# Performance work log

Measured on AMD Instinct MI355X. Metric: run time of the kernel, lower is better.

## Reference

```python
import jax, jax.numpy as jnp
import numpy as np

B, S, D, H = 2, 2048, 1024, 16
DK = D // H


def setup_inputs() -> dict:
    key = jax.random.key(0)
    ks = jax.random.split(key, 12)
    sc = 1.0 / np.sqrt(D)
    inp = {
        "q": jax.random.normal(ks[0], (B, S, D), jnp.float32),
        "k": jax.random.normal(ks[1], (B, S, D), jnp.float32),
        "v": jax.random.normal(ks[2], (B, S, D), jnp.float32),
        # causal mask, broadcastable over batch and heads
        "mask": jnp.tril(jnp.ones((S, S), jnp.int32))[None, None],
        "Wq": jax.random.normal(ks[3], (D, D), jnp.float32) * sc,
        "bq": jax.random.normal(ks[4], (D,), jnp.float32) * 0.02,
        "Wk": jax.random.normal(ks[5], (D, D), jnp.float32) * sc,
        "bk": jax.random.normal(ks[6], (D,), jnp.float32) * 0.02,
        "Wv": jax.random.normal(ks[7], (D, D), jnp.float32) * sc,
        "bv": jax.random.normal(ks[8], (D,), jnp.float32) * 0.02,
        "Wo": jax.random.normal(ks[9], (D, D), jnp.float32) * sc,
        "bo": jax.random.normal(ks[10], (D,), jnp.float32) * 0.02,
    }
    return inp


def reference(q, k, v, mask, Wq, bq, Wk, bk, Wv, bv, Wo, bo):
    b, s, _ = q.shape
    # QKV projections (torch Linear: x @ W.T + b)
    qh = (q @ Wq.T + bq).reshape(b, s, H, DK).transpose(0, 2, 1, 3)  # [B,H,S,DK]
    kh = (k @ Wk.T + bk).reshape(b, -1, H, DK).transpose(0, 2, 1, 3)
    vh = (v @ Wv.T + bv).reshape(b, -1, H, DK).transpose(0, 2, 1, 3)
    scores = jnp.einsum("bhqd,bhkd->bhqk", qh, kh) / np.sqrt(DK)  # [B,H,S,S]
    scores = jnp.where(mask == 0, jnp.float32(-1e9), scores)
    attn = jax.nn.softmax(scores, axis=-1)
    # dropout p=0.0 (eval) -> identity
    x = jnp.einsum("bhqk,bhkd->bhqd", attn, vh)  # [B,H,S,DK]
    x = x.transpose(0, 2, 1, 3).reshape(b, s, H * DK)
    return x @ Wo.T + bo
```

## Files before the change

### kernel.cpp

```cpp
#include <hip/hip_runtime.h>
#include <hip/hip_bf16.h>
#include <cstdint>
#include <cstddef>

using u16   = unsigned short;
using u32   = uint32_t;
using u16x4 = __attribute__((ext_vector_type(4))) unsigned short;
using u16x8 = __attribute__((ext_vector_type(8))) unsigned short;
using s16x8 = __attribute__((ext_vector_type(8))) short;
using f32x4 = __attribute__((ext_vector_type(4))) float;
using f32x16 = __attribute__((ext_vector_type(16))) float;

#define B_DIM  2
#define S_DIM  2048
#define D_DIM  1024
#define H_DIM  16
#define DK_DIM 64

__device__ __forceinline__ u16 f2bf(float f) {
  union { float f; uint32_t u; } c; c.f = f;
  uint32_t u = c.u;
  return (u16)((u + 0x7FFFu + ((u >> 16) & 1u)) >> 16);
}
__device__ __forceinline__ float bf2f(u16 v) {
  union { uint32_t u; float f; } c; c.u = (uint32_t)v << 16;
  return c.f;
}

__device__ __forceinline__ void gload16(const void* g, void* l) {
  __builtin_amdgcn_global_load_lds(
      (const __attribute__((address_space(1))) void*)g,
      (__attribute__((address_space(3))) void*)l, 16, 0, 0);
}

__device__ __forceinline__ int chunk_base(int qt) {
  return (qt < 4) ? qt
       : (qt < 8) ? 4 + 2 * (qt - 4)
       : (qt < 12) ? 12 + 3 * (qt - 8)
       : 24 + 4 * (qt - 12);
}

__global__ __launch_bounds__(256) void cast_bf16_kernel(
    const float* s0, const float* s1, const float* s2, const float* s3,
    u16* d0, u16* d1, u16* d2, u16* d3, int n)
{
  const float* s; u16* d;
  switch (blockIdx.y) {
    case 0: s = s0; d = d0; break;
    case 1: s = s1; d = d1; break;
    case 2: s = s2; d = d2; break;
    default: s = s3; d = d3; break;
  }
  int i = (blockIdx.x * 256 + threadIdx.x) * 8;
  if (i >= n) return;
  f32x4 a = *(const f32x4*)(s + i);
  f32x4 b = *(const f32x4*)(s + i + 4);
  u16x8 ov;
  ov[0] = f2bf(a[0]); ov[1] = f2bf(a[1]); ov[2] = f2bf(a[2]); ov[3] = f2bf(a[3]);
  ov[4] = f2bf(b[0]); ov[5] = f2bf(b[1]); ov[6] = f2bf(b[2]); ov[7] = f2bf(b[3]);
  *(u16x8*)(d + i) = ov;
}

#define BM 128
#define BN 128
#define BK 64

__device__ __forceinline__ void gemm_bt_core(
    const u16* __restrict__ A, const u16* __restrict__ W,
    const float* __restrict__ bias, void* __restrict__ out, int mode,
    int mtile, int ntile, float oscale)
{
  __shared__ u16 Alds[BM * BK];
  __shared__ u16 Blds[BN * BK];
  const int K = 1024;
  const int tid = threadIdx.x;
  const int w = tid >> 6, l = tid & 63;
  const int lr = l & 15, lg = l >> 4;
  const int wr = w >> 1, wc = w & 1;
  const int m0 = mtile * BM, n0 = ntile * BN;

  f32x4 acc[4][4] = {};

  for (int kt = 0; kt < K / BK; ++kt) {
    const int k0 = kt * BK;
    #pragma unroll
    for (int i = 0; i < 4; ++i) {
      int c = i * 256 + tid;
      int r = c >> 3;
      int cb = ((c & 7) << 4) ^ ((r & 7) << 4);
      gload16((const char*)(A + (size_t)(m0 + r) * K + k0) + cb,
              (char*)Alds + i * 4096 + w * 1024);
    }
    #pragma unroll
    for (int i = 0; i < 4; ++i) {
      int c = i * 256 + tid;
      int r = c >> 3;
      int cb = ((c & 7) << 4) ^ ((r & 7) << 4);
      gload16((const char*)(W + (size_t)(n0 + r) * K + k0) + cb,
              (char*)Blds + i * 4096 + w * 1024);
    }
    __syncthreads();
    #pragma unroll
    for (int ks = 0; ks < 2; ++ks) {
      s16x8 af[4], bf[4];
      #pragma unroll
      for (int mi = 0; mi < 4; ++mi) {
        int r = wr * 64 + mi * 16 + lr;
        int kb = (ks * 64 + lg * 16) ^ ((r & 7) << 4);
        af[mi] = *(const s16x8*)((const char*)Alds + r * 128 + kb);
      }
      #pragma unroll
      for (int ni = 0; ni < 4; ++ni) {
        int r = wc * 64 + ni * 16 + lr;
        int kb = (ks * 64 + lg * 16) ^ ((r & 7) << 4);
        bf[ni] = *(const s16x8*)((const char*)Blds + r * 128 + kb);
      }
      #pragma unroll
      for (int mi = 0; mi < 4; ++mi)
        #pragma unroll
        for (int ni = 0; ni < 4; ++ni)
          acc[mi][ni] = __builtin_amdgcn_mfma_f32_16x16x32_bf16(
              af[mi], bf[ni], acc[mi][ni], 0, 0, 0);
    }
    __syncthreads();
  }

  const int mbase = m0 + wr * 64 + lg * 4;
  const int nbase = n0 + wc * 64 + lr;
  #pragma unroll
  for (int ni = 0; ni < 4; ++ni) {
    int n = nbase + ni * 16;
    float bb = bias[n];
    #pragma unroll
    for (int mi = 0; mi < 4; ++mi) {
      int mr = mbase + mi * 16;
      f32x4 vv = acc[mi][ni];
      if (mode == 2) {
        float* o = (float*)out;
        #pragma unroll
        for (int r = 0; r < 4; ++r) o[(size_t)(mr + r) * 1024 + n] = vv[r] + bb;
      } else if (mode == 0) {
        u16* o = (u16*)out;
        #pragma unroll
        for (int r = 0; r < 4; ++r)
          o[(size_t)(mr + r) * 1024 + n] = f2bf((vv[r] + bb) * oscale);
      } else {
        u16* o = (u16*)out;
        int b = mr >> 11, s = mr & (S_DIM - 1);
        int h = n >> 6, dk = n & 63;
        u16x4 pk;
        #pragma unroll
        for (int r = 0; r < 4; ++r) pk[r] = f2bf(vv[r] + bb);
        *(u16x4*)(o + ((size_t)((b * H_DIM + h) * DK_DIM + dk) * S_DIM + s)) = pk;
      }
    }
  }
}

__global__ __launch_bounds__(256) void qkv_gemm_kernel(
    const u16* xq, const u16* xk, const u16* xv,
    const u16* wq, const u16* wk, const u16* wv,
    const float* bq, const float* bk, const float* bv,
    u16* qlin, u16* klin, u16* vt)
{
  const int f = blockIdx.x;
  const int xcd = f & 7;
  const int s = f >> 3;
  const int z = s >> 5;
  const int r = s & 31;
  const int mtile = xcd * 4 + (r >> 3);
  const int ntile = r & 7;

  const u16* A = (z == 0) ? xq : (z == 1) ? xk : xv;
  const u16* W = (z == 0) ? wq : (z == 1) ? wk : wv;
  const float* bias = (z == 0) ? bq : (z == 1) ? bk : bv;
  void* out = (z == 0) ? (void*)qlin : (z == 1) ? (void*)klin : (void*)vt;
  gemm_bt_core(A, W, bias, out, (z == 2) ? 1 : 0, mtile, ntile,
               (z == 0) ? 0.125f * 1.44269504f : 1.0f);
}

__global__ __launch_bounds__(256) void oproj_kernel(
    const u16* aout, const u16* wo, const float* bo, float* out)
{
  const int f = blockIdx.x;
  const int xcd = f & 7;
  const int s = f >> 3;
  const int mtile = xcd * 4 + (s >> 3);
  const int ntile = s & 7;
  gemm_bt_core(aout, wo, bo, (void*)out, 2, mtile, ntile, 1.0f);
}

__global__ __launch_bounds__(256, 4) void attn_kernel(
    const u16* __restrict__ qlin, const u16* __restrict__ klin,
    const u16* __restrict__ vt, u16* __restrict__ opart,
    float* __restrict__ lpart)
{
  __shared__ u16 Klds[2][8 * 512];
  __shared__ u16 Vlds[2][8 * 512];
  const int tid = threadIdx.x;
  const int w = tid >> 6, l = tid & 63;
  const int lq = l & 31, hi = l >> 5;

  const int f = blockIdx.x;
  const int bh = f & 31;
  const int g = f >> 5;
  int qt, ch;
  if (g < 16)      { qt = 15 - (g >> 2);        ch = g & 3; }
  else if (g < 28) { qt = 11 - (g - 16) / 3;    ch = (g - 16) % 3; }
  else if (g < 36) { qt = 7 - ((g - 28) >> 1);  ch = (g - 28) & 1; }
  else             { qt = 3 - (g - 36);         ch = 0; }
  const int T  = 2 * qt + 2;
  const int nc = (T + 7) >> 3;
  const int jlo = (ch * T) / nc;
  const int jhi = ((ch + 1) * T) / nc;
  const int b = bh >> 4, h = bh & 15;

  const int qb  = qt * 128 + w * 32;
  const int myq = qb + lq;
  const int jtend_w = (qb + 31) >> 6;

  s16x8 qf[4];
  {
    const u16* qptr = qlin + (size_t)(b * S_DIM + myq) * D_DIM + h * DK_DIM + hi * 8;
    #pragma unroll
    for (int db = 0; db < 4; ++db) qf[db] = *(const s16x8*)(qptr + db * 16);
  }

  const u16* kg = klin + (size_t)b * S_DIM * D_DIM + h * DK_DIM;
  const u16* vg = vt + (size_t)(b * H_DIM + h) * DK_DIM * S_DIM;

  f32x16 o0 = {}, o1 = {};
  float l_run = 0.f;

  auto stage = [&](int buf, int jt) {
    const int j0 = jt * 64;
    #pragma unroll
    for (int i = 0; i < 2; ++i) {
      int fk = w * 2 + i;
      int db = fk >> 1, rh = fk & 1;
      gload16(kg + (size_t)(j0 + rh * 32 + lq) * D_DIM + db * 16 + hi * 8,
              (char*)&Klds[buf][0] + fk * 1024);
      gload16(vg + (size_t)(rh * 32 + lq) * S_DIM + j0 + db * 16 + hi * 8,
              (char*)&Vlds[buf][0] + fk * 1024);
    }
  };

  stage(0, jlo);

  #pragma unroll 1
  for (int jt = jlo; jt < jhi; ++jt) {
    const int cur = (jt - jlo) & 1;
    asm volatile("s_waitcnt vmcnt(0)" ::: "memory");
    __builtin_amdgcn_s_barrier();
    __builtin_amdgcn_sched_barrier(0);
    if (jt + 1 < jhi) stage(cur ^ 1, jt + 1);

    if (jt <= jtend_w) {
      const int j0 = jt * 64;
      const char* Kb = (const char*)&Klds[cur][0];
      const char* Vb = (const char*)&Vlds[cur][0];

      f32x16 s0 = {}, s1 = {};
      #pragma unroll
      for (int db = 0; db < 4; ++db) {
        s16x8 k0 = *(const s16x8*)(Kb + (db * 2 + 0) * 1024 + l * 16);
        s16x8 k1 = *(const s16x8*)(Kb + (db * 2 + 1) * 1024 + l * 16);
        s0 = __builtin_amdgcn_mfma_f32_32x32x16_bf16(k0, qf[db], s0, 0, 0, 0);
        s1 = __builtin_amdgcn_mfma_f32_32x32x16_bf16(k1, qf[db], s1, 0, 0, 0);
      }

      if (j0 + 63 > qb) {
        #pragma unroll
        for (int r = 0; r < 16; ++r) {
          int kr = (r & 3) + 8 * (r >> 2) + 4 * hi;
          if (j0 + kr > myq)      s0[r] = -1e30f;
          if (j0 + 32 + kr > myq) s1[r] = -1e30f;
        }
      }

      u32 wds[16];
      float ls = 0.f;
      #pragma unroll
      for (int i = 0; i < 8; ++i) {
        float pa = __builtin_amdgcn_exp2f(s0[2 * i]);
        float pb = __builtin_amdgcn_exp2f(s0[2 * i + 1]);
        ls += pa + pb;
        wds[i] = (u32)f2bf(pa) | ((u32)f2bf(pb) << 16);
        float pc = __builtin_amdgcn_exp2f(s1[2 * i]);
        float pd = __builtin_amdgcn_exp2f(s1[2 * i + 1]);
        ls += pc + pd;
        wds[8 + i] = (u32)f2bf(pc) | ((u32)f2bf(pd) << 16);
      }
      l_run += ls;

      #pragma unroll
      for (int ks = 0; ks < 4; ++ks) {
        u32 w0 = wds[4 * ks], w1 = wds[4 * ks + 1];
        u32 w2 = wds[4 * ks + 2], w3 = wds[4 * ks + 3];
        u32 ta = __shfl_xor(hi ? w0 : w2, 32);
        u32 tb = __shfl_xor(hi ? w1 : w3, 32);
        union { u32 u[4]; s16x8 v; } pf;
        pf.u[0] = hi ? ta : w0;
        pf.u[1] = hi ? tb : w1;
        pf.u[2] = hi ? w2 : ta;
        pf.u[3] = hi ? w3 : tb;
        s16x8 v0 = *(const s16x8*)(Vb + (ks * 2 + 0) * 1024 + l * 16);
        s16x8 v1 = *(const s16x8*)(Vb + (ks * 2 + 1) * 1024 + l * 16);
        o0 = __builtin_amdgcn_mfma_f32_32x32x16_bf16(v0, pf.v, o0, 0, 0, 0);
        o1 = __builtin_amdgcn_mfma_f32_32x32x16_bf16(v1, pf.v, o1, 0, 0, 0);
      }
    }
  }

  const size_t gslot = (size_t)bh * 40 + chunk_base(qt) + ch;
  u16* ob = opart + ((gslot * 128) + w * 32 + lq) * 64;
  #pragma unroll
  for (int rq = 0; rq < 4; ++rq) {
    u16x4 pk0, pk1;
    #pragma unroll
    for (int j = 0; j < 4; ++j) {
      pk0[j] = f2bf(o0[rq * 4 + j]);
      pk1[j] = f2bf(o1[rq * 4 + j]);
    }
    *(u16x4*)(ob + rq * 8 + hi * 4)      = pk0;
    *(u16x4*)(ob + 32 + rq * 8 + hi * 4) = pk1;
  }
  float lt = l_run + __shfl_xor(l_run, 32);
  if (hi == 0) lpart[gslot * 128 + w * 32 + lq] = lt;
}

__global__ __launch_bounds__(256) void attn_combine_kernel(
    const u16* __restrict__ opart, const float* __restrict__ lpart,
    u16* __restrict__ aout)
{
  const int f = blockIdx.x;
  const int bh = f & 31, qt = f >> 5;
  const int b = bh >> 4, h = bh & 15;
  const int nc = (2 * qt + 9) >> 3;
  const int cs = chunk_base(qt);

  const int t = threadIdx.x;
  const int row = t >> 1, dbase = (t & 1) * 32;
  float acc[32] = {};
  float lsum = 0.f;
  for (int c = 0; c < nc; ++c) {
    const size_t slot = (size_t)bh * 40 + cs + c;
    const u16* pr = opart + ((slot * 128) + row) * 64 + dbase;
    #pragma unroll
    for (int v4 = 0; v4 < 4; ++v4) {
      u16x8 vv = *(const u16x8*)(pr + v4 * 8);
      #pragma unroll
      for (int j = 0; j < 8; ++j) acc[v4 * 8 + j] += bf2f(vv[j]);
    }
    lsum += lpart[slot * 128 + row];
  }
  float inv = 1.f / lsum;
  u16* orow = aout + ((size_t)b * S_DIM + qt * 128 + row) * D_DIM + h * 64 + dbase;
  #pragma unroll
  for (int v4 = 0; v4 < 4; ++v4) {
    u16x8 ov;
    #pragma unroll
    for (int j = 0; j < 8; ++j) ov[j] = f2bf(acc[v4 * 8 + j] * inv);
    *(u16x8*)(orow + v4 * 8) = ov;
  }
}

extern "C" void kernel_launch(void* const* d_in, const int* in_sizes, int n_in,
                              void* d_out, int out_size, void* d_ws, size_t ws_size,
                              hipStream_t stream)
{
  (void)in_sizes; (void)n_in; (void)out_size; (void)ws_size;
  const float* q  = (const float*)d_in[0];
  const float* k  = (const float*)d_in[1];
  const float* v  = (const float*)d_in[2];
  const float* Wq = (const float*)d_in[4];
  const float* bq = (const float*)d_in[5];
  const float* Wk = (const float*)d_in[6];
  const float* bk = (const float*)d_in[7];
  const float* Wv = (const float*)d_in[8];
  const float* bv = (const float*)d_in[9];
  const float* Wo = (const float*)d_in[10];
  const float* bo = (const float*)d_in[11];
  float* out = (float*)d_out;

  const size_t XSZ = (size_t)B_DIM * S_DIM * D_DIM;
  const size_t WSZ = (size_t)D_DIM * D_DIM;

  u16* p = (u16*)d_ws;
  u16* qbf  = p; p += XSZ;
  u16* kbf  = p; p += XSZ;
  u16* vbf  = p; p += XSZ;
  u16* wqb  = p; p += WSZ;
  u16* wkb  = p; p += WSZ;
  u16* wvb  = p; p += WSZ;
  u16* wob  = p; p += WSZ;
  u16* qlin = p; p += XSZ;
  u16* klin = p; p += XSZ;
  u16* vtb  = p; p += XSZ;
  u16* aoutb = p; p += XSZ;

  u16*   opart = (u16*)d_ws;
  float* lpart = (float*)((char*)d_ws + (size_t)1280 * 128 * 64 * 2);

  cast_bf16_kernel<<<dim3((unsigned)(XSZ / 8 / 256), 3), 256, 0, stream>>>(
      q, k, v, nullptr, qbf, kbf, vbf, nullptr, (int)XSZ);
  cast_bf16_kernel<<<dim3((unsigned)(WSZ / 8 / 256), 4), 256, 0, stream>>>(
      Wq, Wk, Wv, Wo, wqb, wkb, wvb, wob, (int)WSZ);
  qkv_gemm_kernel<<<768, 256, 0, stream>>>(
      qbf, kbf, vbf, wqb, wkb, wvb, bq, bk, bv, qlin, klin, vtb);
  attn_kernel<<<1280, 256, 0, stream>>>(qlin, klin, vtb, opart, lpart);
  attn_combine_kernel<<<512, 256, 0, stream>>>(opart, lpart, aoutb);
  oproj_kernel<<<256, 256, 0, stream>>>(aoutb, wob, bo, out);
}
```

Before: 134.3 us.

## Double-buffer GEMM LDS with fragment-major layout and K-step of 32

```diff
diff --git a/kernel.cpp b/kernel.cpp
--- a/kernel.cpp
+++ b/kernel.cpp
@@ -63,16 +63,16 @@
 
 #define BM 128
 #define BN 128
-#define BK 64
 
 __device__ __forceinline__ void gemm_bt_core(
     const u16* __restrict__ A, const u16* __restrict__ W,
     const float* __restrict__ bias, void* __restrict__ out, int mode,
     int mtile, int ntile, float oscale)
 {
-  __shared__ u16 Alds[BM * BK];
-  __shared__ u16 Blds[BN * BK];
+  __shared__ u16 Afr[2][8 * 512];
+  __shared__ u16 Wfr[2][8 * 512];
   const int K = 1024;
+  const int NT = K / 32;
   const int tid = threadIdx.x;
   const int w = tid >> 6, l = tid & 63;
   const int lr = l & 15, lg = l >> 4;
@@ -81,48 +81,45 @@
 
   f32x4 acc[4][4] = {};
 
-  for (int kt = 0; kt < K / BK; ++kt) {
-    const int k0 = kt * BK;
+  auto stage = [&](int buf, int kt) {
+    const int k0 = kt * 32;
     #pragma unroll
     for (int i = 0; i < 4; ++i) {
-      int c = i * 256 + tid;
-      int r = c >> 3;
-      int cb = ((c & 7) << 4) ^ ((r & 7) << 4);
-      gload16((const char*)(A + (size_t)(m0 + r) * K + k0) + cb,
-              (char*)Alds + i * 4096 + w * 1024);
-    }
-    #pragma unroll
-    for (int i = 0; i < 4; ++i) {
-      int c = i * 256 + tid;
-      int r = c >> 3;
-      int cb = ((c & 7) << 4) ^ ((r & 7) << 4);
-      gload16((const char*)(W + (size_t)(n0 + r) * K + k0) + cb,
-              (char*)Blds + i * 4096 + w * 1024);
-    }
-    __syncthreads();
-    #pragma unroll
-    for (int ks = 0; ks < 2; ++ks) {
-      s16x8 af[4], bf[4];
+      int fid = w * 4 + i;
+      if (fid < 8) {
+        gload16(A + (size_t)(m0 + fid * 16 + lr) * K + k0 + lg * 8,
+                (char*)&Afr[buf][fid * 512]);
+      } else {
+        int fb = fid - 8;
+        gload16(W + (size_t)(n0 + fb * 16 + lr) * K + k0 + lg * 8,
+                (char*)&Wfr[buf][fb * 512]);
+      }
+    }
+  };
+
+  stage(0, 0);
+
+  #pragma unroll 1
+  for (int kt = 0; kt < NT; ++kt) {
+    const int cur = kt & 1;
+    asm volatile("s_waitcnt vmcnt(0)" ::: "memory");
+    __builtin_amdgcn_s_barrier();
+    __builtin_amdgcn_sched_barrier(0);
+    if (kt + 1 < NT) stage(cur ^ 1, kt + 1);
+
+    s16x8 af[4], bf[4];
+    #pragma unroll
+    for (int mi = 0; mi < 4; ++mi)
+      af[mi] = *(const s16x8*)(&Afr[cur][(wr * 4 + mi) * 512] + (size_t)l * 8);
+    #pragma unroll
+    for (int ni = 0; ni < 4; ++ni)
+      bf[ni] = *(const s16x8*)(&Wfr[cur][(wc * 4 + ni) * 512] + (size_t)l * 8);
+    #pragma unroll
+    for (int mi = 0; mi < 4; ++mi)
       #pragma unroll
-      for (int mi = 0; mi < 4; ++mi) {
-        int r = wr * 64 + mi * 16 + lr;
-        int kb = (ks * 64 + lg * 16) ^ ((r & 7) << 4);
-        af[mi] = *(const s16x8*)((const char*)Alds + r * 128 + kb);
-      }
-      #pragma unroll
-      for (int ni = 0; ni < 4; ++ni) {
-        int r = wc * 64 + ni * 16 + lr;
-        int kb = (ks * 64 + lg * 16) ^ ((r & 7) << 4);
-        bf[ni] = *(const s16x8*)((const char*)Blds + r * 128 + kb);
-      }
-      #pragma unroll
-      for (int mi = 0; mi < 4; ++mi)
-        #pragma unroll
-        for (int ni = 0; ni < 4; ++ni)
-          acc[mi][ni] = __builtin_amdgcn_mfma_f32_16x16x32_bf16(
-              af[mi], bf[ni], acc[mi][ni], 0, 0, 0);
-    }
-    __syncthreads();
+      for (int ni = 0; ni < 4; ++ni)
+        acc[mi][ni] = __builtin_amdgcn_mfma_f32_16x16x32_bf16(
+            af[mi], bf[ni], acc[mi][ni], 0, 0, 0);
   }
 
   const int mbase = m0 + wr * 64 + lg * 4;
@@ -157,7 +154,7 @@
   }
 }
 
-__global__ __launch_bounds__(256) void qkv_gemm_kernel(
+__global__ __launch_bounds__(256, 4) void qkv_gemm_kernel(
     const u16* xq, const u16* xk, const u16* xv,
     const u16* wq, const u16* wk, const u16* wv,
     const float* bq, const float* bk, const float* bv,
@@ -179,7 +176,7 @@
                (z == 0) ? 0.125f * 1.44269504f : 1.0f);
 }
 
-__global__ __launch_bounds__(256) void oproj_kernel(
+__global__ __launch_bounds__(256, 4) void oproj_kernel(
     const u16* aout, const u16* wo, const float* bo, float* out)
 {
   const int f = blockIdx.x;
```

After: 145.3 us. 1.08x slower.

## Store K and V in MFMA fragment order and load directly to registers

Applied to the files above, without the earlier changes.

```diff
diff --git a/kernel.cpp b/kernel.cpp
--- a/kernel.cpp
+++ b/kernel.cpp
@@ -144,14 +144,30 @@
         #pragma unroll
         for (int r = 0; r < 4; ++r)
           o[(size_t)(mr + r) * 1024 + n] = f2bf((vv[r] + bb) * oscale);
+      } else if (mode == 3) {
+        u16* o = (u16*)out;
+        int h = n >> 6, d = n & 63;
+        int db = d >> 4, hi8 = (d >> 3) & 1, e = d & 7;
+        int bb_ = mr >> 11, j = mr & (S_DIM - 1);
+        int jt = j >> 6, rh = (j >> 5) & 1, lq0 = j & 31;
+        size_t base = (((size_t)(bb_ * H_DIM + h) * 32 + jt) * 8 + (db * 2 + rh))
+                      * 512 + (size_t)(hi8 * 32) * 8 + e;
+        #pragma unroll
+        for (int r = 0; r < 4; ++r)
+          o[base + (size_t)(lq0 + r) * 8] = f2bf(vv[r] + bb);
       } else {
         u16* o = (u16*)out;
-        int b = mr >> 11, s = mr & (S_DIM - 1);
         int h = n >> 6, dk = n & 63;
+        int rh = dk >> 5, lq = dk & 31;
+        int bb_ = mr >> 11, j = mr & (S_DIM - 1);
+        int jt = j >> 6, jj = j & 63;
+        int db = jj >> 4, hi8 = (jj >> 3) & 1, e0 = jj & 7;
+        size_t base = (((size_t)(bb_ * H_DIM + h) * 32 + jt) * 8 + (db * 2 + rh))
+                      * 512 + (size_t)(hi8 * 32 + lq) * 8 + e0;
         u16x4 pk;
         #pragma unroll
         for (int r = 0; r < 4; ++r) pk[r] = f2bf(vv[r] + bb);
-        *(u16x4*)(o + ((size_t)((b * H_DIM + h) * DK_DIM + dk) * S_DIM + s)) = pk;
+        *(u16x4*)(o + base) = pk;
       }
     }
   }
@@ -161,7 +177,7 @@
     const u16* xq, const u16* xk, const u16* xv,
     const u16* wq, const u16* wk, const u16* wv,
     const float* bq, const float* bk, const float* bv,
-    u16* qlin, u16* klin, u16* vt)
+    u16* qlin, u16* kfragb, u16* vfragb)
 {
   const int f = blockIdx.x;
   const int xcd = f & 7;
@@ -174,8 +190,8 @@
   const u16* A = (z == 0) ? xq : (z == 1) ? xk : xv;
   const u16* W = (z == 0) ? wq : (z == 1) ? wk : wv;
   const float* bias = (z == 0) ? bq : (z == 1) ? bk : bv;
-  void* out = (z == 0) ? (void*)qlin : (z == 1) ? (void*)klin : (void*)vt;
-  gemm_bt_core(A, W, bias, out, (z == 2) ? 1 : 0, mtile, ntile,
+  void* out = (z == 0) ? (void*)qlin : (z == 1) ? (void*)kfragb : (void*)vfragb;
+  gemm_bt_core(A, W, bias, out, (z == 0) ? 0 : (z == 1) ? 3 : 1, mtile, ntile,
                (z == 0) ? 0.125f * 1.44269504f : 1.0f);
 }
 
@@ -191,12 +207,10 @@
 }
 
 __global__ __launch_bounds__(256, 4) void attn_kernel(
-    const u16* __restrict__ qlin, const u16* __restrict__ klin,
-    const u16* __restrict__ vt, u16* __restrict__ opart,
+    const u16* __restrict__ qlin, const u16* __restrict__ kfrag,
+    const u16* __restrict__ vfrag, u16* __restrict__ opart,
     float* __restrict__ lpart)
 {
-  __shared__ u16 Klds[2][8 * 512];
-  __shared__ u16 Vlds[2][8 * 512];
   const int tid = threadIdx.x;
   const int w = tid >> 6, l = tid & 63;
   const int lq = l & 31, hi = l >> 5;
@@ -218,6 +232,7 @@
   const int qb  = qt * 128 + w * 32;
   const int myq = qb + lq;
   const int jtend_w = (qb + 31) >> 6;
+  const int jend = (jhi < jtend_w + 1) ? jhi : (jtend_w + 1);
 
   s16x8 qf[4];
   {
@@ -226,89 +241,69 @@
     for (int db = 0; db < 4; ++db) qf[db] = *(const s16x8*)(qptr + db * 16);
   }
 
-  const u16* kg = klin + (size_t)b * S_DIM * D_DIM + h * DK_DIM;
-  const u16* vg = vt + (size_t)(b * H_DIM + h) * DK_DIM * S_DIM;
-
   f32x16 o0 = {}, o1 = {};
   float l_run = 0.f;
 
-  auto stage = [&](int buf, int jt) {
+  #pragma unroll 1
+  for (int jt = jlo; jt < jend; ++jt) {
     const int j0 = jt * 64;
-    #pragma unroll
-    for (int i = 0; i < 2; ++i) {
-      int fk = w * 2 + i;
-      int db = fk >> 1, rh = fk & 1;
-      gload16(kg + (size_t)(j0 + rh * 32 + lq) * D_DIM + db * 16 + hi * 8,
-              (char*)&Klds[buf][0] + fk * 1024);
-      gload16(vg + (size_t)(rh * 32 + lq) * S_DIM + j0 + db * 16 + hi * 8,
-              (char*)&Vlds[buf][0] + fk * 1024);
-    }
-  };
-
-  stage(0, jlo);
-
-  #pragma unroll 1
-  for (int jt = jlo; jt < jhi; ++jt) {
-    const int cur = (jt - jlo) & 1;
-    asm volatile("s_waitcnt vmcnt(0)" ::: "memory");
-    __builtin_amdgcn_s_barrier();
-    __builtin_amdgcn_sched_barrier(0);
-    if (jt + 1 < jhi) stage(cur ^ 1, jt + 1);
-
-    if (jt <= jtend_w) {
-      const int j0 = jt * 64;
-      const char* Kb = (const char*)&Klds[cur][0];
-      const char* Vb = (const char*)&Vlds[cur][0];
-
-      f32x16 s0 = {}, s1 = {};
+    const u16* kb = kfrag + ((size_t)bh * 32 + jt) * 8 * 512;
+    const u16* vb = vfrag + ((size_t)bh * 32 + jt) * 8 * 512;
+
+    s16x8 kf2[8];
+    #pragma unroll
+    for (int fk = 0; fk < 8; ++fk)
+      kf2[fk] = *(const s16x8*)(kb + fk * 512 + (size_t)l * 8);
+
+    f32x16 s0 = {}, s1 = {};
+    #pragma unroll
+    for (int db = 0; db < 4; ++db) {
+      s0 = __builtin_amdgcn_mfma_f32_32x32x16_bf16(kf2[db * 2 + 0], qf[db], s0, 0, 0, 0);
+      s1 = __builtin_amdgcn_mfma_f32_32x32x16_bf16(kf2[db * 2 + 1], qf[db], s1, 0, 0, 0);
+    }
+
+    s16x8 vf2[8];
+    #pragma unroll
+    for (int fk = 0; fk < 8; ++fk)
+      vf2[fk] = *(const s16x8*)(vb + fk * 512 + (size_t)l * 8);
+
+    if (j0 + 63 > qb) {
       #pragma unroll
-      for (int db = 0; db < 4; ++db) {
-        s16x8 k0 = *(const s16x8*)(Kb + (db * 2 + 0) * 1024 + l * 16);
-        s16x8 k1 = *(const s16x8*)(Kb + (db * 2 + 1) * 1024 + l * 16);
-        s0 = __builtin_amdgcn_mfma_f32_32x32x16_bf16(k0, qf[db], s0, 0, 0, 0);
-        s1 = __builtin_amdgcn_mfma_f32_32x32x16_bf16(k1, qf[db], s1, 0, 0, 0);
+      for (int r = 0; r < 16; ++r) {
+        int kr = (r & 3) + 8 * (r >> 2) + 4 * hi;
+        if (j0 + kr > myq)      s0[r] = -1e30f;
+        if (j0 + 32 + kr > myq) s1[r] = -1e30f;
       }
-
-      if (j0 + 63 > qb) {
-        #pragma unroll
-        for (int r = 0; r < 16; ++r) {
-          int kr = (r & 3) + 8 * (r >> 2) + 4 * hi;
-          if (j0 + kr > myq)      s0[r] = -1e30f;
-          if (j0 + 32 + kr > myq) s1[r] = -1e30f;
-        }
-      }
-
-      u32 wds[16];
-      float ls = 0.f;
-      #pragma unroll
-      for (int i = 0; i < 8; ++i) {
-        float pa = __builtin_amdgcn_exp2f(s0[2 * i]);
-        float pb = __builtin_amdgcn_exp2f(s0[2 * i + 1]);
-        ls += pa + pb;
-        wds[i] = (u32)f2bf(pa) | ((u32)f2bf(pb) << 16);
-        float pc = __builtin_amdgcn_exp2f(s1[2 * i]);
-        float pd = __builtin_amdgcn_exp2f(s1[2 * i + 1]);
-        ls += pc + pd;
-        wds[8 + i] = (u32)f2bf(pc) | ((u32)f2bf(pd) << 16);
-      }
-      l_run += ls;
-
-      #pragma unroll
-      for (int ks = 0; ks < 4; ++ks) {
-        u32 w0 = wds[4 * ks], w1 = wds[4 * ks + 1];
-        u32 w2 = wds[4 * ks + 2], w3 = wds[4 * ks + 3];
-        u32 ta = __shfl_xor(hi ? w0 : w2, 32);
-        u32 tb = __shfl_xor(hi ? w1 : w3, 32);
-        union { u32 u[4]; s16x8 v; } pf;
-        pf.u[0] = hi ? ta : w0;
-        pf.u[1] = hi ? tb : w1;
-        pf.u[2] = hi ? w2 : ta;
-        pf.u[3] = hi ? w3 : tb;
-        s16x8 v0 = *(const s16x8*)(Vb + (ks * 2 + 0) * 1024 + l * 16);
-        s16x8 v1 = *(const s16x8*)(Vb + (ks * 2 + 1) * 1024 + l * 16);
-        o0 = __builtin_amdgcn_mfma_f32_32x32x16_bf16(v0, pf.v, o0, 0, 0, 0);
-        o1 = __builtin_amdgcn_mfma_f32_32x32x16_bf16(v1, pf.v, o1, 0, 0, 0);
-      }
+    }
+
+    u32 wds[16];
+    float ls = 0.f;
+    #pragma unroll
+    for (int i = 0; i < 8; ++i) {
+      float pa = __builtin_amdgcn_exp2f(s0[2 * i]);
+      float pb = __builtin_amdgcn_exp2f(s0[2 * i + 1]);
+      ls += pa + pb;
+      wds[i] = (u32)f2bf(pa) | ((u32)f2bf(pb) << 16);
+      float pc = __builtin_amdgcn_exp2f(s1[2 * i]);
+      float pd = __builtin_amdgcn_exp2f(s1[2 * i + 1]);
+      ls += pc + pd;
+      wds[8 + i] = (u32)f2bf(pc) | ((u32)f2bf(pd) << 16);
+    }
+    l_run += ls;
+
+    #pragma unroll
+    for (int ks = 0; ks < 4; ++ks) {
+      u32 w0 = wds[4 * ks], w1 = wds[4 * ks + 1];
+      u32 w2 = wds[4 * ks + 2], w3 = wds[4 * ks + 3];
+      u32 ta = __shfl_xor(hi ? w0 : w2, 32);
+      u32 tb = __shfl_xor(hi ? w1 : w3, 32);
+      union { u32 u[4]; s16x8 v; } pf;
+      pf.u[0] = hi ? ta : w0;
+      pf.u[1] = hi ? tb : w1;
+      pf.u[2] = hi ? w2 : ta;
+      pf.u[3] = hi ? w3 : tb;
+      o0 = __builtin_amdgcn_mfma_f32_32x32x16_bf16(vf2[ks * 2 + 0], pf.v, o0, 0, 0, 0);
+      o1 = __builtin_amdgcn_mfma_f32_32x32x16_bf16(vf2[ks * 2 + 1], pf.v, o1, 0, 0, 0);
     }
   }
 
@@ -394,10 +389,10 @@
   u16* wkb  = p; p += WSZ;
   u16* wvb  = p; p += WSZ;
   u16* wob  = p; p += WSZ;
-  u16* qlin = p; p += XSZ;
-  u16* klin = p; p += XSZ;
-  u16* vtb  = p; p += XSZ;
-  u16* aoutb = p; p += XSZ;
+  u16* qlin   = p; p += XSZ;
+  u16* kfragb = p; p += XSZ;
+  u16* vfragb = p; p += XSZ;
+  u16* aoutb  = p; p += XSZ;
 
   u16*   opart = (u16*)d_ws;
   float* lpart = (float*)((char*)d_ws + (size_t)1280 * 128 * 64 * 2);
@@ -407,8 +402,8 @@
   cast_bf16_kernel<<<dim3((unsigned)(WSZ / 8 / 256), 4), 256, 0, stream>>>(
       Wq, Wk, Wv, Wo, wqb, wkb, wvb, wob, (int)WSZ);
   qkv_gemm_kernel<<<768, 256, 0, stream>>>(
-      qbf, kbf, vbf, wqb, wkb, wvb, bq, bk, bv, qlin, klin, vtb);
-  attn_kernel<<<1280, 256, 0, stream>>>(qlin, klin, vtb, opart, lpart);
+      qbf, kbf, vbf, wqb, wkb, wvb, bq, bk, bv, qlin, kfragb, vfragb);
+  attn_kernel<<<1280, 256, 0, stream>>>(qlin, kfragb, vfragb, opart, lpart);
   attn_combine_kernel<<<512, 256, 0, stream>>>(opart, lpart, aoutb);
   oproj_kernel<<<256, 256, 0, stream>>>(aoutb, wob, bo, out);
 }
```

After: 135.0 us. About the same (+0.5%).
